# Kernel optimization log

Hardware: AMD Instinct MI355X
Metric: run time of the kernel (lower is better)

Reference implementation:

```python
import jax, jax.numpy as jnp
import numpy as np

GMIN = 0.01
GMAX = 10.0


def _ptanh(x, eta):
    # printed tanh-style learnable activation: eta0 + eta1 * tanh((x - eta2) * eta3)
    return eta[0] + eta[1] * jnp.tanh((x - eta[2]) * eta[3])


def setup_inputs() -> dict:
    key = jax.random.key(0)
    k1, k2 = jax.random.split(key)
    B, n_in, n_out = 32768, 256, 256
    a_previous = jax.random.uniform(k1, (B, n_in), dtype=jnp.float32)
    eta_act = jnp.array([0.0, 1.0, 0.5, 2.0], dtype=jnp.float32)
    eta_inv = jnp.array([1.0, -1.0, 0.5, 2.0], dtype=jnp.float32)
    # theta init exactly as in pLayer.__init__
    theta = jax.random.uniform(k2, (n_in + 2, n_out), dtype=jnp.float32) / 100.0 + GMIN
    theta = theta.at[-1, :].add(GMAX)
    ratio = eta_act[2] / (1.0 - eta_act[2])  # eta2/(1-eta2)
    theta = theta.at[-2, :].set(ratio * (jnp.sum(theta[:-2, :], axis=0) + theta[-1, :]))
    return {"a_previous": a_previous, "theta_": theta, "eta_act": eta_act, "eta_inv": eta_inv}


def reference(a_previous, theta_, eta_act, eta_inv):
    # clamp + threshold-to-zero (forward value of the straight-through theta)
    theta = jnp.clip(theta_, -GMAX, GMAX)
    theta = jnp.where(jnp.abs(theta) < GMIN, 0.0, theta)
    # normalized conductance weights
    abs_t = jnp.abs(theta)
    W = abs_t / jnp.sum(abs_t, axis=0, keepdims=True)  # [n_in+2, n_out]
    pos = (theta >= 0.0).astype(theta.dtype)
    neg = 1.0 - pos
    B = a_previous.shape[0]
    ones = jnp.ones((B, 1), dtype=a_previous.dtype)
    zeros = jnp.zeros((B, 1), dtype=a_previous.dtype)
    a_ext = jnp.concatenate([a_previous, ones, zeros], axis=1)  # [B, n_in+2]
    a_neg = _ptanh(a_ext, eta_inv).at[:, -1].set(0.0)  # inverter, last (dummy) col zeroed
    z = a_ext @ (W * pos) + a_neg @ (W * neg)  # [B, n_out]
    return _ptanh(z, eta_act)
```

## Files before the change

### kernel.cpp

```cpp
#include <hip/hip_runtime.h>
#include <hip/hip_bf16.h>

typedef unsigned int u32;
typedef __attribute__((ext_vector_type(8))) _Float16 f16x8;
typedef __attribute__((ext_vector_type(4))) float f32x4;

#define GMIN_ 0.01f
#define GMAX_ 10.0f
#define LOG2E_ 1.4426950408889634f

__device__ __forceinline__ float tanh_exp2(float y2l) {
    float e = __builtin_amdgcn_exp2f(y2l);
    float r = __builtin_amdgcn_rcpf(e + 1.0f);
    return fmaf(-2.0f, r, 1.0f);
}

__global__ __launch_bounds__(256) void prep_weights(
    const float* __restrict__ theta, const float* __restrict__ eta_inv,
    _Float16* __restrict__ W2t, float* __restrict__ bias)
{
    __shared__ float tile[258][17];
    __shared__ float psum[16][17];
    __shared__ float cinv[16];

    const int t  = threadIdx.x;
    const int kq = t >> 4;
    const int nl = t & 15;
    const int n  = blockIdx.x * 16 + nl;

    float part = 0.f;
#pragma unroll
    for (int i = 0; i < 17; ++i) {
        const int k = i * 16 + kq;
        if (k < 258) {
            float tt = theta[k * 256 + n];
            tt = fminf(fmaxf(tt, -GMAX_), GMAX_);
            if (fabsf(tt) < GMIN_) tt = 0.f;
            tile[k][nl] = tt;
            part += fabsf(tt);
        }
    }
    psum[kq][nl] = part;
    __syncthreads();
    if (kq == 0) {
        float s = 0.f;
#pragma unroll
        for (int j = 0; j < 16; ++j) s += psum[j][nl];
        cinv[nl] = 1.0f / s;
    }
    __syncthreads();

    const int nw = t >> 4;
    const int kc = t & 15;
    const float inv = cinv[nw];
    const int nn = blockIdx.x * 16 + nw;
#pragma unroll
    for (int c = 0; c < 4; ++c) {
        f16x8 h;
#pragma unroll
        for (int e = 0; e < 4; ++e) {
            const float tt = tile[kc * 16 + c * 4 + e][nw];
            const float w  = fabsf(tt) * inv;
            const float wp = (tt >= 0.f) ? w : 0.f;
            h[2 * e]     = (_Float16)wp;
            h[2 * e + 1] = (_Float16)(w - wp);
        }
        *(f16x8*)(W2t + (size_t)nn * 512 + kc * 32 + c * 8) = h;
    }

    if (t < 16) {
        const float tt = tile[256][t];
        const float w  = fabsf(tt) * cinv[t];
        const float wp = (tt >= 0.f) ? w : 0.f;
        const float wn = w - wp;
        const float ei0 = eta_inv[0], ei1 = eta_inv[1], ei2 = eta_inv[2], ei3 = eta_inv[3];
        const float a1  = ei0 + ei1 * tanhf((1.0f - ei2) * ei3);
        bias[blockIdx.x * 16 + t] = wp + a1 * wn;
    }
}

__global__ __launch_bounds__(256, 4) void plax_gemm(
    const float* __restrict__ A, const _Float16* __restrict__ W2t,
    const float* __restrict__ bias, const float* __restrict__ eta_act,
    const float* __restrict__ eta_inv, float* __restrict__ out)
{
    __shared__ __align__(16) char Bs[2][16384];

    const int t    = threadIdx.x;
    const int bid  = blockIdx.x;
    const int swz  = ((bid & 7) << 7) | (bid >> 3);
    const int mblk = swz >> 2;
    const int nblk = swz & 3;
    const int lane = t & 63, wave = t >> 6;
    const int lr   = lane & 15, lg = lane >> 4;

    const float ei0 = eta_inv[0], ei1 = eta_inv[1];
    const float k2i = 2.0f * eta_inv[3] * LOG2E_;
    const float c2i = 2.0f * eta_inv[2] * eta_inv[3] * LOG2E_;

    const int row0 = mblk * 128 + wave * 32;
    const int col0 = nblk * 64;

    const float* ap = A + (size_t)(row0 + lr) * 256 + lg * 4;

    const char* bsrc = (const char*)W2t
        + (size_t)(col0 + (t >> 4)) * 1024
        + (size_t)(((t & 15) ^ (t >> 4)) * 16);

    f32x4 acc[2][4] = {};
    float4 aq[4][2];

#define LDA(it_) do {                                               \
        aq[(it_) & 3][0] = *(const float4*)(ap + (it_) * 16);       \
        aq[(it_) & 3][1] = *(const float4*)(ap + 4096 + (it_) * 16);\
    } while (0)

#define STAGE_B(r_, bb_) do {                                                   \
        _Pragma("unroll")                                                       \
        for (int i_ = 0; i_ < 4; ++i_)                                          \
            __builtin_amdgcn_global_load_lds(                                   \
                (const __attribute__((address_space(1))) u32*)                  \
                    (bsrc + (size_t)i_ * 16384 + (size_t)(r_) * 256),           \
                (__attribute__((address_space(3))) u32*)                        \
                    ((char*)Bs + (bb_) * 16384 + i_ * 4096 + t * 16),           \
                16, 0, 0);                                                      \
    } while (0)

    STAGE_B(0, 0);
    asm volatile("s_waitcnt vmcnt(0)" ::: "memory");
    __builtin_amdgcn_sched_barrier(0);
    __builtin_amdgcn_s_barrier();
    LDA(0); LDA(1); LDA(2);

#pragma unroll
    for (int r = 0; r < 4; ++r) {
        if (r < 3) STAGE_B(r + 1, (r + 1) & 1);

        const char* buf = (const char*)Bs + (r & 1) * 16384;
#pragma unroll
        for (int j = 0; j < 4; ++j) {
            const int it = r * 4 + j;
            if (it + 3 < 16) LDA(it + 3);

            const float4* acur = aq[it & 3];
            f16x8 af[2];
#pragma unroll
            for (int m = 0; m < 2; ++m) {
                const float4 v = acur[m];
                f16x8 h;
                h[0] = (_Float16)v.x;
                h[1] = (_Float16)fmaf(ei1, tanh_exp2(fmaf(v.x, k2i, -c2i)), ei0);
                h[2] = (_Float16)v.y;
                h[3] = (_Float16)fmaf(ei1, tanh_exp2(fmaf(v.y, k2i, -c2i)), ei0);
                h[4] = (_Float16)v.z;
                h[5] = (_Float16)fmaf(ei1, tanh_exp2(fmaf(v.z, k2i, -c2i)), ei0);
                h[6] = (_Float16)v.w;
                h[7] = (_Float16)fmaf(ei1, tanh_exp2(fmaf(v.w, k2i, -c2i)), ei0);
                af[m] = h;
            }

            f16x8 bf[4];
#pragma unroll
            for (int n = 0; n < 4; ++n) {
                const int rr   = n * 16 + lr;
                const int phys = (j * 4 + lg) ^ lr;
                bf[n] = *(const f16x8*)(buf + rr * 256 + phys * 16);
            }

#pragma unroll
            for (int m = 0; m < 2; ++m)
#pragma unroll
                for (int n = 0; n < 4; ++n)
                    acc[m][n] = __builtin_amdgcn_mfma_f32_16x16x32_f16(
                        af[m], bf[n], acc[m][n], 0, 0, 0);
        }

        if (r < 3) {
            asm volatile("s_waitcnt vmcnt(0)" ::: "memory");
            __builtin_amdgcn_sched_barrier(0);
            __builtin_amdgcn_s_barrier();
        }
    }
#undef LDA
#undef STAGE_B

    const float ea0 = eta_act[0], ea1 = eta_act[1];
    const float k2a = 2.0f * eta_act[3] * LOG2E_;
    const float c2a = 2.0f * eta_act[2] * eta_act[3] * LOG2E_;

    float bc[4];
#pragma unroll
    for (int n = 0; n < 4; ++n) bc[n] = bias[col0 + n * 16 + lr];

#pragma unroll
    for (int m = 0; m < 2; ++m) {
        const int rgb = row0 + m * 16 + lg * 4;
#pragma unroll
        for (int n = 0; n < 4; ++n) {
            const int cg = col0 + n * 16 + lr;
#pragma unroll
            for (int j = 0; j < 4; ++j) {
                const float z = acc[m][n][j] + bc[n];
                out[(size_t)(rgb + j) * 256 + cg] =
                    fmaf(ea1, tanh_exp2(fmaf(z, k2a, -c2a)), ea0);
            }
        }
    }
}

extern "C" void kernel_launch(void* const* d_in, const int* in_sizes, int n_in,
                              void* d_out, int out_size, void* d_ws, size_t ws_size,
                              hipStream_t stream) {
    (void)in_sizes; (void)n_in; (void)out_size; (void)ws_size;
    const float* a       = (const float*)d_in[0];
    const float* theta   = (const float*)d_in[1];
    const float* eta_act = (const float*)d_in[2];
    const float* eta_inv = (const float*)d_in[3];
    float* out = (float*)d_out;

    _Float16* W2t  = (_Float16*)d_ws;
    float*    bias = (float*)((char*)d_ws + 256 * 512 * 2);

    prep_weights<<<16, 256, 0, stream>>>(theta, eta_inv, W2t, bias);
    plax_gemm<<<1024, 256, 0, stream>>>(a, W2t, bias, eta_act, eta_inv, out);
}
```

Before: 107.1 us.

## Fuse weight preparation into GEMM kernel, building fp16 weight tiles per block

Removes the separate prep_weights launch. Each GEMM block now reads theta directly, computes the column normalisation sums and bias itself, and packs pos/neg fp16 weights into double-buffered LDS between k-chunks. This removes one kernel launch and the workspace round trip. In exchange, all 1024 blocks redundantly read a full 258x64 theta slice and do the column reduction, with strided scalar loads and extra barriers. The A prefetch depth also drops from 3 to 2 iterations, likely to save registers for the theta staging.

```diff
diff --git a/kernel.cpp b/kernel.cpp
--- a/kernel.cpp
+++ b/kernel.cpp
@@ -15,76 +15,20 @@
     return fmaf(-2.0f, r, 1.0f);
 }
 
-__global__ __launch_bounds__(256) void prep_weights(
-    const float* __restrict__ theta, const float* __restrict__ eta_inv,
-    _Float16* __restrict__ W2t, float* __restrict__ bias)
-{
-    __shared__ float tile[258][17];
-    __shared__ float psum[16][17];
-    __shared__ float cinv[16];
-
-    const int t  = threadIdx.x;
-    const int kq = t >> 4;
-    const int nl = t & 15;
-    const int n  = blockIdx.x * 16 + nl;
-
-    float part = 0.f;
-#pragma unroll
-    for (int i = 0; i < 17; ++i) {
-        const int k = i * 16 + kq;
-        if (k < 258) {
-            float tt = theta[k * 256 + n];
-            tt = fminf(fmaxf(tt, -GMAX_), GMAX_);
-            if (fabsf(tt) < GMIN_) tt = 0.f;
-            tile[k][nl] = tt;
-            part += fabsf(tt);
-        }
-    }
-    psum[kq][nl] = part;
-    __syncthreads();
-    if (kq == 0) {
-        float s = 0.f;
-#pragma unroll
-        for (int j = 0; j < 16; ++j) s += psum[j][nl];
-        cinv[nl] = 1.0f / s;
-    }
-    __syncthreads();
-
-    const int nw = t >> 4;
-    const int kc = t & 15;
-    const float inv = cinv[nw];
-    const int nn = blockIdx.x * 16 + nw;
-#pragma unroll
-    for (int c = 0; c < 4; ++c) {
-        f16x8 h;
-#pragma unroll
-        for (int e = 0; e < 4; ++e) {
-            const float tt = tile[kc * 16 + c * 4 + e][nw];
-            const float w  = fabsf(tt) * inv;
-            const float wp = (tt >= 0.f) ? w : 0.f;
-            h[2 * e]     = (_Float16)wp;
-            h[2 * e + 1] = (_Float16)(w - wp);
-        }
-        *(f16x8*)(W2t + (size_t)nn * 512 + kc * 32 + c * 8) = h;
-    }
-
-    if (t < 16) {
-        const float tt = tile[256][t];
-        const float w  = fabsf(tt) * cinv[t];
-        const float wp = (tt >= 0.f) ? w : 0.f;
-        const float wn = w - wp;
-        const float ei0 = eta_inv[0], ei1 = eta_inv[1], ei2 = eta_inv[2], ei3 = eta_inv[3];
-        const float a1  = ei0 + ei1 * tanhf((1.0f - ei2) * ei3);
-        bias[blockIdx.x * 16 + t] = wp + a1 * wn;
-    }
-}
-
-__global__ __launch_bounds__(256, 4) void plax_gemm(
-    const float* __restrict__ A, const _Float16* __restrict__ W2t,
-    const float* __restrict__ bias, const float* __restrict__ eta_act,
-    const float* __restrict__ eta_inv, float* __restrict__ out)
+__device__ __forceinline__ float clamp_thresh(float tt) {
+    tt = fminf(fmaxf(tt, -GMAX_), GMAX_);
+    return (fabsf(tt) < GMIN_) ? 0.f : tt;
+}
+
+__global__ __launch_bounds__(256, 4) void plax_fused(
+    const float* __restrict__ A, const float* __restrict__ theta,
+    const float* __restrict__ eta_act, const float* __restrict__ eta_inv,
+    float* __restrict__ out)
 {
     __shared__ __align__(16) char Bs[2][16384];
+    __shared__ float psum[4][64];
+    __shared__ float sinv[64];
+    __shared__ float sbias[64];
 
     const int t    = threadIdx.x;
     const int bid  = blockIdx.x;
@@ -93,56 +37,89 @@
     const int nblk = swz & 3;
     const int lane = t & 63, wave = t >> 6;
     const int lr   = lane & 15, lg = lane >> 4;
-
-    const float ei0 = eta_inv[0], ei1 = eta_inv[1];
-    const float k2i = 2.0f * eta_inv[3] * LOG2E_;
-    const float c2i = 2.0f * eta_inv[2] * eta_inv[3] * LOG2E_;
+    const int cl   = t & 63;
+    const int sg   = t >> 6;
+
+    const float ei0 = eta_inv[0], ei1 = eta_inv[1], ei2 = eta_inv[2], ei3 = eta_inv[3];
+    const float k2i = 2.0f * ei3 * LOG2E_;
+    const float c2i = 2.0f * ei2 * ei3 * LOG2E_;
 
     const int row0 = mblk * 128 + wave * 32;
     const int col0 = nblk * 64;
 
     const float* ap = A + (size_t)(row0 + lr) * 256 + lg * 4;
-
-    const char* bsrc = (const char*)W2t
-        + (size_t)(col0 + (t >> 4)) * 1024
-        + (size_t)(((t & 15) ^ (t >> 4)) * 16);
+    const float* thc = theta + col0 + cl;
 
     f32x4 acc[2][4] = {};
-    float4 aq[4][2];
-
-#define LDA(it_) do {                                               \
-        aq[(it_) & 3][0] = *(const float4*)(ap + (it_) * 16);       \
-        aq[(it_) & 3][1] = *(const float4*)(ap + 4096 + (it_) * 16);\
+    float4 aq[3][2];
+
+#define LDA(it_) do {                                                \
+        aq[(it_) % 3][0] = *(const float4*)(ap + (it_) * 16);        \
+        aq[(it_) % 3][1] = *(const float4*)(ap + 4096 + (it_) * 16); \
     } while (0)
 
-#define STAGE_B(r_, bb_) do {                                                   \
-        _Pragma("unroll")                                                       \
-        for (int i_ = 0; i_ < 4; ++i_)                                          \
-            __builtin_amdgcn_global_load_lds(                                   \
-                (const __attribute__((address_space(1))) u32*)                  \
-                    (bsrc + (size_t)i_ * 16384 + (size_t)(r_) * 256),           \
-                (__attribute__((address_space(3))) u32*)                        \
-                    ((char*)Bs + (bb_) * 16384 + i_ * 4096 + t * 16),           \
-                16, 0, 0);                                                      \
+    float tth[16];
+#define LOAD_TH(r_) do {                                             \
+        _Pragma("unroll")                                            \
+        for (int q_ = 0; q_ < 16; ++q_)                              \
+            tth[q_] = thc[((r_) * 64 + sg * 16 + q_) * 256];         \
     } while (0)
 
-    STAGE_B(0, 0);
-    asm volatile("s_waitcnt vmcnt(0)" ::: "memory");
+#define PACK_WRITE(bb_, inv_) do {                                   \
+        _Pragma("unroll")                                            \
+        for (int si_ = 0; si_ < 4; ++si_) {                          \
+            f16x8 h_;                                                \
+            _Pragma("unroll")                                        \
+            for (int e_ = 0; e_ < 4; ++e_) {                         \
+                const float tt_ = clamp_thresh(tth[si_ * 4 + e_]);   \
+                const float w_  = fabsf(tt_) * (inv_);               \
+                const float wp_ = (tt_ >= 0.f) ? w_ : 0.f;           \
+                h_[2 * e_]     = (_Float16)wp_;                      \
+                h_[2 * e_ + 1] = (_Float16)(w_ - wp_);               \
+            }                                                        \
+            *(f16x8*)((char*)Bs + (bb_) * 16384 + cl * 256           \
+                      + (((sg * 4 + si_) ^ (cl & 15)) * 16)) = h_;   \
+        }                                                            \
+    } while (0)
+
+    LDA(0); LDA(1);
+
+    float part = 0.f;
+    for (int k = sg; k < 258; k += 4)
+        part += fabsf(clamp_thresh(thc[k * 256]));
+    psum[sg][cl] = part;
+
+    LOAD_TH(0);
+    __syncthreads();
+    if (t < 64) {
+        const float s  = psum[0][t] + psum[1][t] + psum[2][t] + psum[3][t];
+        const float iv = 1.0f / s;
+        sinv[t] = iv;
+        const float t6 = clamp_thresh(theta[256 * 256 + col0 + t]);
+        const float w6 = fabsf(t6) * iv;
+        const float wp = (t6 >= 0.f) ? w6 : 0.f;
+        const float a1 = ei0 + ei1 * tanh_exp2((1.0f - ei2) * ei3 * 2.0f * LOG2E_);
+        sbias[t] = wp + a1 * (w6 - wp);
+    }
+    __syncthreads();
+    const float inv = sinv[cl];
+
+    PACK_WRITE(0, inv);
+    asm volatile("s_waitcnt lgkmcnt(0)" ::: "memory");
     __builtin_amdgcn_sched_barrier(0);
     __builtin_amdgcn_s_barrier();
-    LDA(0); LDA(1); LDA(2);
 
 #pragma unroll
     for (int r = 0; r < 4; ++r) {
-        if (r < 3) STAGE_B(r + 1, (r + 1) & 1);
+        if (r < 3) LOAD_TH(r + 1);
 
         const char* buf = (const char*)Bs + (r & 1) * 16384;
 #pragma unroll
         for (int j = 0; j < 4; ++j) {
             const int it = r * 4 + j;
-            if (it + 3 < 16) LDA(it + 3);
-
-            const float4* acur = aq[it & 3];
+            if (it + 2 < 16) LDA(it + 2);
+
+            const float4* acur = aq[it % 3];
             f16x8 af[2];
 #pragma unroll
             for (int m = 0; m < 2; ++m) {
@@ -176,13 +153,16 @@
         }
 
         if (r < 3) {
-            asm volatile("s_waitcnt vmcnt(0)" ::: "memory");
+            __builtin_amdgcn_s_barrier();
+            PACK_WRITE((r + 1) & 1, inv);
+            asm volatile("s_waitcnt lgkmcnt(0)" ::: "memory");
             __builtin_amdgcn_sched_barrier(0);
             __builtin_amdgcn_s_barrier();
         }
     }
 #undef LDA
-#undef STAGE_B
+#undef LOAD_TH
+#undef PACK_WRITE
 
     const float ea0 = eta_act[0], ea1 = eta_act[1];
     const float k2a = 2.0f * eta_act[3] * LOG2E_;
@@ -190,7 +170,7 @@
 
     float bc[4];
 #pragma unroll
-    for (int n = 0; n < 4; ++n) bc[n] = bias[col0 + n * 16 + lr];
+    for (int n = 0; n < 4; ++n) bc[n] = sbias[n * 16 + lr];
 
 #pragma unroll
     for (int m = 0; m < 2; ++m) {
@@ -211,16 +191,12 @@
 extern "C" void kernel_launch(void* const* d_in, const int* in_sizes, int n_in,
                               void* d_out, int out_size, void* d_ws, size_t ws_size,
                               hipStream_t stream) {
-    (void)in_sizes; (void)n_in; (void)out_size; (void)ws_size;
+    (void)in_sizes; (void)n_in; (void)out_size; (void)d_ws; (void)ws_size;
     const float* a       = (const float*)d_in[0];
     const float* theta   = (const float*)d_in[1];
     const float* eta_act = (const float*)d_in[2];
     const float* eta_inv = (const float*)d_in[3];
     float* out = (float*)d_out;
 
-    _Float16* W2t  = (_Float16*)d_ws;
-    float*    bias = (float*)((char*)d_ws + 256 * 512 * 2);
-
-    prep_weights<<<16, 256, 0, stream>>>(theta, eta_inv, W2t, bias);
-    plax_gemm<<<1024, 256, 0, stream>>>(a, W2t, bias, eta_act, eta_inv, out);
-}
+    plax_fused<<<1024, 256, 0, stream>>>(a, theta, eta_act, eta_inv, out);
+}
```

New measurement: 118.1 us. 1.1x slower.
